# Kernel tuning notes

Measured on AMD Instinct MI355X. Metric: run time of the kernel, lower is better.

Reference implementation:

```python
import jax, jax.numpy as jnp
import numpy as np

N = 40000
E = 640000
IN_C = 128
HID = 256
HEADS = 8


def _gat(x, W, att_src, att_dst, bias, src, dst, num_nodes, heads, concat):
    # x: [N, Fin], W: [Fin, heads*C], att_*: [heads, C], bias: [out_dim]
    xp = (x @ W).reshape(num_nodes, heads, -1)          # [N, H, C]
    a_s = jnp.sum(xp * att_src, axis=-1)                # [N, H]
    a_d = jnp.sum(xp * att_dst, axis=-1)                # [N, H]
    e = jax.nn.leaky_relu(a_s[src] + a_d[dst], 0.2)     # [E, H]
    # per-destination-node softmax over incoming edges (self-loops guarantee >=1)
    m = jax.ops.segment_max(e, dst, num_segments=num_nodes)
    m = jnp.where(jnp.isfinite(m), m, 0.0)
    ex = jnp.exp(e - m[dst])
    denom = jax.ops.segment_sum(ex, dst, num_segments=num_nodes)
    alpha = ex / (denom[dst] + 1e-16)                   # [E, H]
    out = jax.ops.segment_sum(xp[src] * alpha[..., None], dst, num_segments=num_nodes)  # [N,H,C]
    out = out.reshape(num_nodes, -1) if concat else out.mean(axis=1)
    return out + bias


def setup_inputs() -> dict:
    key = jax.random.key(0)
    ks = jax.random.split(key, 16)
    C = HID // HEADS
    s = 0.05
    return {
        "x": jax.random.normal(ks[0], (N, IN_C), jnp.float32),
        "edge_index": jax.random.randint(ks[1], (2, E), 0, N, jnp.int32),
        "W0": jax.random.normal(ks[2], (IN_C, HEADS * C), jnp.float32) * s,
        "att_s0": jax.random.normal(ks[3], (HEADS, C), jnp.float32) * s,
        "att_d0": jax.random.normal(ks[4], (HEADS, C), jnp.float32) * s,
        "b0": jnp.zeros((HID,), jnp.float32),
        # BatchNorm(256)
        "gamma0": jnp.ones((HID,), jnp.float32),
        "beta0": jnp.zeros((HID,), jnp.float32),
        # skip projection Linear(128 -> 256)
        "W_skip": jax.random.normal(ks[5], (IN_C, HID), jnp.float32) * s,
        "b_skip": jnp.zeros((HID,), jnp.float32),
        # last layer: GATConv(256 -> 256, heads=1, concat=False)
        "W1": jax.random.normal(ks[6], (HID, HID), jnp.float32) * s,
        "att_s1": jax.random.normal(ks[7], (1, HID), jnp.float32) * s,
        "att_d1": jax.random.normal(ks[8], (1, HID), jnp.float32) * s,
        "b1": jnp.zeros((HID,), jnp.float32),
    }


def reference(x, edge_index, W0, att_s0, att_d0, b0, gamma0, beta0,
              W_skip, b_skip, W1, att_s1, att_d1, b1):
    loops = jnp.arange(N, dtype=edge_index.dtype)
    src = jnp.concatenate([edge_index[0], loops])
    dst = jnp.concatenate([edge_index[1], loops])
    # conv 0 (heads=8, concat)
    h = _gat(x, W0, att_s0, att_d0, b0, src, dst, N, HEADS, True)
    # BatchNorm (training-style batch stats, biased variance, eps=1e-5)
    mu = h.mean(axis=0)
    var = h.var(axis=0)
    h = (h - mu) / jnp.sqrt(var + 1e-5) * gamma0 + beta0
    h = jax.nn.elu(h)
    # dropout is identity in eval mode
    # residual: shapes differ (128 vs 256) -> skip_proj(x_initial) + h at i==0
    h = h + (x @ W_skip + b_skip)
    # conv 1 (heads=1, concat=False -> mean over single head)
    out = _gat(h, W1, att_s1, att_d1, b1, src, dst, N, 1, False)
    return out
```

## Files before the change

### kernel.cpp

```cpp
#include <hip/hip_runtime.h>
#include <hip/hip_bf16.h>

#define NN 40000
#define EE 640000
#define ET 680000
#define MPAD 40064
#define LOG2E 1.4426950408889634f

typedef __attribute__((ext_vector_type(8))) short short8;
typedef __attribute__((ext_vector_type(4))) float f32x4;

__device__ __forceinline__ float bf2f(unsigned u) {
    return __uint_as_float(u << 16);
}
__device__ __forceinline__ unsigned short f2bf(float f) {
    unsigned u = __float_as_uint(f);
    return (unsigned short)((u + 0x7FFFu + ((u >> 16) & 1u)) >> 16);
}
__device__ __forceinline__ unsigned pack2(float lo, float hi) {
    return ((unsigned)f2bf(lo)) | (((unsigned)f2bf(hi)) << 16);
}
__device__ __forceinline__ void unpack2(unsigned u, float& lo, float& hi) {
    lo = __uint_as_float(u << 16);
    hi = __uint_as_float(u & 0xffff0000u);
}

__global__ __launch_bounds__(256) void conv_x(const float* __restrict__ x,
                                              unsigned short* __restrict__ xb)
{
    int i = blockIdx.x * 256 + threadIdx.x;
    if (i >= MPAD * 128 / 4) return;
    int row = (i * 4) >> 7;
    ushort4 o;
    if (row < NN) {
        float4 v = ((const float4*)x)[i];
        o.x = f2bf(v.x); o.y = f2bf(v.y); o.z = f2bf(v.z); o.w = f2bf(v.w);
    } else { o.x = o.y = o.z = o.w = 0; }
    ((ushort4*)xb)[i] = o;
}

__global__ __launch_bounds__(256) void conv_wt_all(
    const float* __restrict__ W0, const float* __restrict__ Ws,
    const float* __restrict__ W1, unsigned short* __restrict__ Wtc,
    unsigned short* __restrict__ W1t)
{
    int i = blockIdx.x * 256 + threadIdx.x;
    if (i < 32768) {
        int c = i >> 7, k = i & 127;
        Wtc[i] = f2bf(W0[(size_t)k * 256 + c]);
    } else if (i < 65536) {
        int j = i - 32768;
        int c = j >> 7, k = j & 127;
        Wtc[i] = f2bf(Ws[(size_t)k * 256 + c]);
    } else if (i < 131072) {
        int j = i - 65536;
        int c = j >> 8, k = j & 255;
        W1t[j] = f2bf(W1[(size_t)k * 256 + c]);
    }
}

__global__ __launch_bounds__(256) void gemm_bf16(
    const unsigned short* __restrict__ A, const unsigned short* __restrict__ Btc,
    unsigned short* __restrict__ C0, unsigned short* __restrict__ C1, int K)
{
    __shared__ unsigned short As[128 * 64];
    int tid = threadIdx.x;
    int rb = blockIdx.x * 128, cb = blockIdx.y * 128;
    int lane = tid & 63, wid = tid >> 6;
    int wm = (wid >> 1) * 64, wn = (wid & 1) * 64;
    int lr = lane & 15, lk = lane >> 4;
    f32x4 acc[4][4] = {};
    for (int kb = 0; kb < K; kb += 64) {
        #pragma unroll
        for (int i = 0; i < 4; i++) {
            int flat = tid + i * 256;
            int r = flat >> 3, c8 = flat & 7;
            int4 v = *(const int4*)(A + (size_t)(rb + r) * K + kb + c8 * 8);
            *(int4*)(&As[r * 64 + ((c8 ^ (r & 7)) * 8)]) = v;
        }
        __syncthreads();
        #pragma unroll
        for (int kk = 0; kk < 2; kk++) {
            int kbase = kb + kk * 32 + lk * 8;
            short8 bfr[4], afr[4];
            #pragma unroll
            for (int n = 0; n < 4; n++)
                bfr[n] = *(const short8*)(Btc + (size_t)(cb + wn + n * 16 + lr) * K + kbase);
            #pragma unroll
            for (int m = 0; m < 4; m++) {
                int row = wm + m * 16 + lr;
                int kchunk = kk * 4 + lk;
                afr[m] = *(const short8*)(&As[row * 64 + ((kchunk ^ (row & 7)) * 8)]);
            }
            #pragma unroll
            for (int m = 0; m < 4; m++)
                #pragma unroll
                for (int n = 0; n < 4; n++)
                    acc[m][n] = __builtin_amdgcn_mfma_f32_16x16x32_bf16(afr[m], bfr[n], acc[m][n], 0, 0, 0);
        }
        __syncthreads();
    }
    unsigned short* C = (cb < 256) ? C0 : C1;
    int cbase = cb & 255;
    #pragma unroll
    for (int m = 0; m < 4; m++)
        #pragma unroll
        for (int n = 0; n < 4; n++) {
            int col = cbase + wn + n * 16 + lr;
            #pragma unroll
            for (int j = 0; j < 4; j++) {
                int row = rb + wm + m * 16 + lk * 4 + j;
                C[(size_t)row * 256 + col] = f2bf(acc[m][n][j]);
            }
        }
}

__global__ __launch_bounds__(256) void csr_count(const int* __restrict__ ei, int* __restrict__ deg)
{
    int e = blockIdx.x * blockDim.x + threadIdx.x;
    if (e >= ET) return;
    int d = (e < EE) ? ei[EE + e] : (e - EE);
    atomicAdd(&deg[d], 1);
}

__global__ __launch_bounds__(1024) void exscan(
    const int* __restrict__ deg, int* __restrict__ rowptr, int* __restrict__ cursor)
{
    __shared__ int wsum[16];
    __shared__ int carry_s;
    int tid = threadIdx.x, lane = tid & 63, wid = tid >> 6;
    if (tid == 0) carry_s = 0;
    __syncthreads();
    for (int base = 0; base < NN; base += 1024) {
        int i = base + tid;
        int v = (i < NN) ? deg[i] : 0;
        int sc = v;
        #pragma unroll
        for (int off = 1; off < 64; off <<= 1) {
            int t = __shfl_up(sc, off);
            if (lane >= off) sc += t;
        }
        if (lane == 63) wsum[wid] = sc;
        __syncthreads();
        if (wid == 0 && lane < 16) {
            int t = wsum[lane];
            #pragma unroll
            for (int off = 1; off < 16; off <<= 1) {
                int u = __shfl_up(t, off);
                if (lane >= off) t += u;
            }
            wsum[lane] = t;
        }
        __syncthreads();
        int carry = carry_s;
        int wpre = wid ? wsum[wid - 1] : 0;
        int excl = carry + wpre + sc - v;
        if (i < NN) { rowptr[i] = excl; cursor[i] = excl; }
        __syncthreads();
        if (tid == 0) carry_s = carry + wsum[15];
    }
    if (tid == 0) rowptr[NN] = carry_s;
}

__global__ __launch_bounds__(256) void csr_fill(
    const int* __restrict__ ei, int* __restrict__ cursor, int* __restrict__ adj)
{
    int e = blockIdx.x * blockDim.x + threadIdx.x;
    if (e >= ET) return;
    int s, d;
    if (e < EE) { s = ei[e]; d = ei[EE + e]; } else { s = d = e - EE; }
    int pos = atomicAdd(&cursor[d], 1);
    adj[pos] = s;
}

__global__ __launch_bounds__(256) void attn_node0(
    const unsigned short* __restrict__ xp, const float* __restrict__ att_s,
    const float* __restrict__ att_d, float* __restrict__ a_s, float* __restrict__ a_d)
{
    int t = blockIdx.x * 256 + threadIdx.x;
    if (t >= NN * 8) return;
    int n = t >> 3, h = t & 7;
    const unsigned short* p = xp + (size_t)n * 256 + h * 32;
    float s = 0.f, dd = 0.f;
    #pragma unroll
    for (int i0 = 0; i0 < 32; i0 += 8) {
        uint4 raw = *(const uint4*)(p + i0);
        unsigned vals[4] = {raw.x, raw.y, raw.z, raw.w};
        #pragma unroll
        for (int q = 0; q < 4; q++) {
            float lo, hi;
            unpack2(vals[q], lo, hi);
            s  += lo * att_s[h * 32 + i0 + q * 2] + hi * att_s[h * 32 + i0 + q * 2 + 1];
            dd += lo * att_d[h * 32 + i0 + q * 2] + hi * att_d[h * 32 + i0 + q * 2 + 1];
        }
    }
    a_s[t] = s * LOG2E; a_d[t] = dd * LOG2E;
}

__global__ __launch_bounds__(256) void attn_node1(
    const unsigned short* __restrict__ xp, const float* __restrict__ att_s,
    const float* __restrict__ att_d, float* __restrict__ a_s, float* __restrict__ a_d)
{
    int w = (blockIdx.x * 256 + threadIdx.x) >> 6;
    int lane = threadIdx.x & 63;
    if (w >= NN) return;
    ushort4 raw = ((const ushort4*)(xp + (size_t)w * 256))[lane];
    float4 a = ((const float4*)att_s)[lane];
    float4 b = ((const float4*)att_d)[lane];
    float v0 = bf2f(raw.x), v1 = bf2f(raw.y), v2 = bf2f(raw.z), v3 = bf2f(raw.w);
    float s  = v0 * a.x + v1 * a.y + v2 * a.z + v3 * a.w;
    float dd = v0 * b.x + v1 * b.y + v2 * b.z + v3 * b.w;
    #pragma unroll
    for (int off = 32; off; off >>= 1) {
        s  += __shfl_down(s, off);
        dd += __shfl_down(dd, off);
    }
    if (lane == 0) { a_s[w] = s * LOG2E; a_d[w] = dd * LOG2E; }
}

__global__ __launch_bounds__(256) void gather0(
    const int* __restrict__ adj, const int* __restrict__ rowptr,
    const unsigned short* __restrict__ xp, const float* __restrict__ a_s,
    const float* __restrict__ a_d, unsigned short* __restrict__ out0)
{
    int w = (blockIdx.x * 256 + threadIdx.x) >> 6;
    int lane = threadIdx.x & 63;
    if (w >= NN) return;
    int hl = lane & 31;
    int hw = lane >> 5;
    int h = hl >> 2;
    float ad = a_d[w * 8 + h];
    int p = rowptr[w], end = rowptr[w + 1];
    unsigned loff = (unsigned)hl * 16u;
    float a0=0,a1=0,a2=0,a3=0,a4=0,a5=0,a6=0,a7=0;
    float b0=0,b1=0,b2=0,b3=0,b4=0,b5=0,b6=0,b7=0;
    float den0 = 0.f, den1 = 0.f;
    float lo, hi;
    for (; p + 8 <= end; p += 8) {
        int sA = adj[p + hw];
        int sB = adj[p + 2 + hw];
        int sC = adj[p + 4 + hw];
        int sD = adj[p + 6 + hw];
        float eA = a_s[sA * 8 + h] + ad;
        float eB = a_s[sB * 8 + h] + ad;
        float eC = a_s[sC * 8 + h] + ad;
        float eD = a_s[sD * 8 + h] + ad;
        float wA = __builtin_amdgcn_exp2f(fmaxf(eA, 0.2f * eA));
        float wB = __builtin_amdgcn_exp2f(fmaxf(eB, 0.2f * eB));
        float wC = __builtin_amdgcn_exp2f(fmaxf(eC, 0.2f * eC));
        float wD = __builtin_amdgcn_exp2f(fmaxf(eD, 0.2f * eD));
        uint4 rA = *(const uint4*)((const char*)xp + ((unsigned)sA * 512u + loff));
        uint4 rB = *(const uint4*)((const char*)xp + ((unsigned)sB * 512u + loff));
        uint4 rC = *(const uint4*)((const char*)xp + ((unsigned)sC * 512u + loff));
        uint4 rD = *(const uint4*)((const char*)xp + ((unsigned)sD * 512u + loff));
        den0 += wA + wC; den1 += wB + wD;
        unpack2(rA.x, lo, hi); a0 += wA * lo; a1 += wA * hi;
        unpack2(rA.y, lo, hi); a2 += wA * lo; a3 += wA * hi;
        unpack2(rA.z, lo, hi); a4 += wA * lo; a5 += wA * hi;
        unpack2(rA.w, lo, hi); a6 += wA * lo; a7 += wA * hi;
        unpack2(rB.x, lo, hi); b0 += wB * lo; b1 += wB * hi;
        unpack2(rB.y, lo, hi); b2 += wB * lo; b3 += wB * hi;
        unpack2(rB.z, lo, hi); b4 += wB * lo; b5 += wB * hi;
        unpack2(rB.w, lo, hi); b6 += wB * lo; b7 += wB * hi;
        unpack2(rC.x, lo, hi); a0 += wC * lo; a1 += wC * hi;
        unpack2(rC.y, lo, hi); a2 += wC * lo; a3 += wC * hi;
        unpack2(rC.z, lo, hi); a4 += wC * lo; a5 += wC * hi;
        unpack2(rC.w, lo, hi); a6 += wC * lo; a7 += wC * hi;
        unpack2(rD.x, lo, hi); b0 += wD * lo; b1 += wD * hi;
        unpack2(rD.y, lo, hi); b2 += wD * lo; b3 += wD * hi;
        unpack2(rD.z, lo, hi); b4 += wD * lo; b5 += wD * hi;
        unpack2(rD.w, lo, hi); b6 += wD * lo; b7 += wD * hi;
    }
    for (; p + 2 <= end; p += 2) {
        int sA = adj[p + hw];
        float eA = a_s[sA * 8 + h] + ad;
        float wA = __builtin_amdgcn_exp2f(fmaxf(eA, 0.2f * eA));
        uint4 rA = *(const uint4*)((const char*)xp + ((unsigned)sA * 512u + loff));
        den0 += wA;
        unpack2(rA.x, lo, hi); a0 += wA * lo; a1 += wA * hi;
        unpack2(rA.y, lo, hi); a2 += wA * lo; a3 += wA * hi;
        unpack2(rA.z, lo, hi); a4 += wA * lo; a5 += wA * hi;
        unpack2(rA.w, lo, hi); a6 += wA * lo; a7 += wA * hi;
    }
    if (p < end) {
        int sA = adj[p];
        float eA = a_s[sA * 8 + h] + ad;
        float wA = hw ? 0.f : __builtin_amdgcn_exp2f(fmaxf(eA, 0.2f * eA));
        uint4 rA = *(const uint4*)((const char*)xp + ((unsigned)sA * 512u + loff));
        den0 += wA;
        unpack2(rA.x, lo, hi); a0 += wA * lo; a1 += wA * hi;
        unpack2(rA.y, lo, hi); a2 += wA * lo; a3 += wA * hi;
        unpack2(rA.z, lo, hi); a4 += wA * lo; a5 += wA * hi;
        unpack2(rA.w, lo, hi); a6 += wA * lo; a7 += wA * hi;
    }
    a0 += b0; a1 += b1; a2 += b2; a3 += b3;
    a4 += b4; a5 += b5; a6 += b6; a7 += b7;
    float den = den0 + den1;
    den += __shfl_xor(den, 32);
    a0 += __shfl_xor(a0, 32); a1 += __shfl_xor(a1, 32);
    a2 += __shfl_xor(a2, 32); a3 += __shfl_xor(a3, 32);
    a4 += __shfl_xor(a4, 32); a5 += __shfl_xor(a5, 32);
    a6 += __shfl_xor(a6, 32); a7 += __shfl_xor(a7, 32);
    if (hw == 0) {
        float inv = 1.f / (den + 1e-16f);
        uint4 o;
        o.x = pack2(a0 * inv, a1 * inv);
        o.y = pack2(a2 * inv, a3 * inv);
        o.z = pack2(a4 * inv, a5 * inv);
        o.w = pack2(a6 * inv, a7 * inv);
        *(uint4*)((char*)out0 + ((size_t)w * 512u + loff)) = o;
    }
}

__global__ __launch_bounds__(256) void bn_stats(
    const unsigned short* __restrict__ H, float* __restrict__ bnsum, float* __restrict__ bnsq)
{
    int c = threadIdx.x;
    int r0 = blockIdx.x * 64;
    float s = 0.f, sq = 0.f;
    for (int r = r0; r < r0 + 64; r++) {
        float v = bf2f(H[(size_t)r * 256 + c]);
        s += v; sq += v * v;
    }
    atomicAdd(&bnsum[c], s);
    atomicAdd(&bnsq[c], sq);
}

__global__ __launch_bounds__(256) void bn_elu(
    const unsigned short* __restrict__ out0, unsigned short* __restrict__ hb,
    const float* __restrict__ bnsum, const float* __restrict__ bnsq,
    const float* __restrict__ gamma, const float* __restrict__ beta,
    const float* __restrict__ bskip)
{
    int i = blockIdx.x * 256 + threadIdx.x;
    if (i >= MPAD * 256 / 8) return;
    int col0 = (i * 8) & 255;
    uint4 hv = ((const uint4*)out0)[i];
    uint4 sv = ((const uint4*)hb)[i];
    float bn[8], sk[8];
    unpack2(hv.x, bn[0], bn[1]); unpack2(hv.y, bn[2], bn[3]);
    unpack2(hv.z, bn[4], bn[5]); unpack2(hv.w, bn[6], bn[7]);
    unpack2(sv.x, sk[0], sk[1]); unpack2(sv.y, sk[2], sk[3]);
    unpack2(sv.z, sk[4], sk[5]); unpack2(sv.w, sk[6], sk[7]);
    const float invN = 1.0f / (float)NN;
    float r[8];
    #pragma unroll
    for (int q = 0; q < 8; q++) {
        int c = col0 + q;
        float mu = bnsum[c] * invN;
        float var = bnsq[c] * invN - mu * mu;
        float scl = rsqrtf(var + 1e-5f) * gamma[c];
        float b = (bn[q] - mu) * scl + beta[c];
        float el = b > 0.f ? b : (__expf(b) - 1.f);
        r[q] = el + sk[q] + bskip[c];
    }
    uint4 o;
    o.x = pack2(r[0], r[1]); o.y = pack2(r[2], r[3]);
    o.z = pack2(r[4], r[5]); o.w = pack2(r[6], r[7]);
    ((uint4*)hb)[i] = o;
}

__global__ __launch_bounds__(256) void gather1(
    const int* __restrict__ adj, const int* __restrict__ rowptr,
    const unsigned short* __restrict__ xp, const float* __restrict__ a_s,
    const float* __restrict__ a_d, const float* __restrict__ b1,
    float* __restrict__ out)
{
    int w = (blockIdx.x * 256 + threadIdx.x) >> 6;
    int lane = threadIdx.x & 63;
    if (w >= NN) return;
    int hl = lane & 31;
    int hw = lane >> 5;
    float ad = a_d[w];
    int p = rowptr[w], end = rowptr[w + 1];
    unsigned loff = (unsigned)hl * 16u;
    float a0=0,a1=0,a2=0,a3=0,a4=0,a5=0,a6=0,a7=0;
    float b0s=0,b1s=0,b2s=0,b3s=0,b4s=0,b5s=0,b6s=0,b7s=0;
    float den0 = 0.f, den1 = 0.f;
    float lo, hi;
    for (; p + 8 <= end; p += 8) {
        int sA = adj[p + hw];
        int sB = adj[p + 2 + hw];
        int sC = adj[p + 4 + hw];
        int sD = adj[p + 6 + hw];
        float eA = a_s[sA] + ad;
        float eB = a_s[sB] + ad;
        float eC = a_s[sC] + ad;
        float eD = a_s[sD] + ad;
        float wA = __builtin_amdgcn_exp2f(fmaxf(eA, 0.2f * eA));
        float wB = __builtin_amdgcn_exp2f(fmaxf(eB, 0.2f * eB));
        float wC = __builtin_amdgcn_exp2f(fmaxf(eC, 0.2f * eC));
        float wD = __builtin_amdgcn_exp2f(fmaxf(eD, 0.2f * eD));
        uint4 rA = *(const uint4*)((const char*)xp + ((unsigned)sA * 512u + loff));
        uint4 rB = *(const uint4*)((const char*)xp + ((unsigned)sB * 512u + loff));
        uint4 rC = *(const uint4*)((const char*)xp + ((unsigned)sC * 512u + loff));
        uint4 rD = *(const uint4*)((const char*)xp + ((unsigned)sD * 512u + loff));
        den0 += wA + wC; den1 += wB + wD;
        unpack2(rA.x, lo, hi); a0 += wA * lo; a1 += wA * hi;
        unpack2(rA.y, lo, hi); a2 += wA * lo; a3 += wA * hi;
        unpack2(rA.z, lo, hi); a4 += wA * lo; a5 += wA * hi;
        unpack2(rA.w, lo, hi); a6 += wA * lo; a7 += wA * hi;
        unpack2(rB.x, lo, hi); b0s += wB * lo; b1s += wB * hi;
        unpack2(rB.y, lo, hi); b2s += wB * lo; b3s += wB * hi;
        unpack2(rB.z, lo, hi); b4s += wB * lo; b5s += wB * hi;
        unpack2(rB.w, lo, hi); b6s += wB * lo; b7s += wB * hi;
        unpack2(rC.x, lo, hi); a0 += wC * lo; a1 += wC * hi;
        unpack2(rC.y, lo, hi); a2 += wC * lo; a3 += wC * hi;
        unpack2(rC.z, lo, hi); a4 += wC * lo; a5 += wC * hi;
        unpack2(rC.w, lo, hi); a6 += wC * lo; a7 += wC * hi;
        unpack2(rD.x, lo, hi); b0s += wD * lo; b1s += wD * hi;
        unpack2(rD.y, lo, hi); b2s += wD * lo; b3s += wD * hi;
        unpack2(rD.z, lo, hi); b4s += wD * lo; b5s += wD * hi;
        unpack2(rD.w, lo, hi); b6s += wD * lo; b7s += wD * hi;
    }
    for (; p + 2 <= end; p += 2) {
        int sA = adj[p + hw];
        float eA = a_s[sA] + ad;
        float wA = __builtin_amdgcn_exp2f(fmaxf(eA, 0.2f * eA));
        uint4 rA = *(const uint4*)((const char*)xp + ((unsigned)sA * 512u + loff));
        den0 += wA;
        unpack2(rA.x, lo, hi); a0 += wA * lo; a1 += wA * hi;
        unpack2(rA.y, lo, hi); a2 += wA * lo; a3 += wA * hi;
        unpack2(rA.z, lo, hi); a4 += wA * lo; a5 += wA * hi;
        unpack2(rA.w, lo, hi); a6 += wA * lo; a7 += wA * hi;
    }
    if (p < end) {
        int sA = adj[p];
        float eA = a_s[sA] + ad;
        float wA = hw ? 0.f : __builtin_amdgcn_exp2f(fmaxf(eA, 0.2f * eA));
        uint4 rA = *(const uint4*)((const char*)xp + ((unsigned)sA * 512u + loff));
        den0 += wA;
        unpack2(rA.x, lo, hi); a0 += wA * lo; a1 += wA * hi;
        unpack2(rA.y, lo, hi); a2 += wA * lo; a3 += wA * hi;
        unpack2(rA.z, lo, hi); a4 += wA * lo; a5 += wA * hi;
        unpack2(rA.w, lo, hi); a6 += wA * lo; a7 += wA * hi;
    }
    a0 += b0s; a1 += b1s; a2 += b2s; a3 += b3s;
    a4 += b4s; a5 += b5s; a6 += b6s; a7 += b7s;
    float den = den0 + den1;
    den += __shfl_xor(den, 32);
    a0 += __shfl_xor(a0, 32); a1 += __shfl_xor(a1, 32);
    a2 += __shfl_xor(a2, 32); a3 += __shfl_xor(a3, 32);
    a4 += __shfl_xor(a4, 32); a5 += __shfl_xor(a5, 32);
    a6 += __shfl_xor(a6, 32); a7 += __shfl_xor(a7, 32);
    if (hw == 0) {
        float inv = 1.f / (den + 1e-16f);
        const float* bb = b1 + hl * 8;
        float4 o0 = {a0 * inv + bb[0], a1 * inv + bb[1],
                     a2 * inv + bb[2], a3 * inv + bb[3]};
        float4 o1 = {a4 * inv + bb[4], a5 * inv + bb[5],
                     a6 * inv + bb[6], a7 * inv + bb[7]};
        float* orow = out + (size_t)w * 256 + hl * 8;
        *(float4*)(orow) = o0;
        *(float4*)(orow + 4) = o1;
    }
}

extern "C" void kernel_launch(void* const* d_in, const int* in_sizes, int n_in,
                              void* d_out, int out_size, void* d_ws, size_t ws_size,
                              hipStream_t stream)
{
    const float* x      = (const float*)d_in[0];
    const int*   ei     = (const int*)d_in[1];
    const float* W0     = (const float*)d_in[2];
    const float* att_s0 = (const float*)d_in[3];
    const float* att_d0 = (const float*)d_in[4];
    const float* gamma0 = (const float*)d_in[6];
    const float* beta0  = (const float*)d_in[7];
    const float* W_skip = (const float*)d_in[8];
    const float* b_skip = (const float*)d_in[9];
    const float* W1     = (const float*)d_in[10];
    const float* att_s1 = (const float*)d_in[11];
    const float* att_d1 = (const float*)d_in[12];
    const float* b1     = (const float*)d_in[13];
    float* out = (float*)d_out;

    char* p = (char*)d_ws;
    unsigned short* x_bf  = (unsigned short*)p; p += (size_t)MPAD * 128 * 2;
    unsigned short* xp_bf = (unsigned short*)p; p += (size_t)MPAD * 256 * 2;
    unsigned short* h_bf  = (unsigned short*)p; p += (size_t)MPAD * 256 * 2;
    unsigned short* out0b = (unsigned short*)p; p += (size_t)MPAD * 256 * 2;
    unsigned short* Wtc   = (unsigned short*)p; p += (size_t)512 * 128 * 2;
    unsigned short* W1t   = (unsigned short*)p; p += (size_t)256 * 256 * 2;
    float* a_s   = (float*)p; p += (size_t)NN * 8 * 4;
    float* a_d   = (float*)p; p += (size_t)NN * 8 * 4;
    float* bnsum = (float*)p; p += 256 * 4;
    float* bnsq  = (float*)p; p += 256 * 4;
    int* deg    = (int*)p; p += (size_t)NN * 4;
    int* rowptr = (int*)p; p += (size_t)(NN + 1) * 4;
    int* cursor = (int*)p; p += (size_t)NN * 4;
    int* adj    = (int*)p; p += (size_t)ET * 4;

    hipMemsetAsync(deg, 0, (size_t)NN * 4, stream);
    hipMemsetAsync(bnsum, 0, 512 * 4, stream);
    hipMemsetAsync(out0b + (size_t)NN * 256, 0, (size_t)(MPAD - NN) * 256 * 2, stream);

    conv_x<<<(MPAD * 128 / 4 + 255) / 256, 256, 0, stream>>>(x, x_bf);
    conv_wt_all<<<(131072 + 255) / 256, 256, 0, stream>>>(W0, W_skip, W1, Wtc, W1t);

    csr_count<<<(ET + 255) / 256, 256, 0, stream>>>(ei, deg);
    exscan<<<1, 1024, 0, stream>>>(deg, rowptr, cursor);
    csr_fill<<<(ET + 255) / 256, 256, 0, stream>>>(ei, cursor, adj);

    dim3 gg0(MPAD / 128, 4);
    gemm_bf16<<<gg0, 256, 0, stream>>>(x_bf, Wtc, xp_bf, h_bf, 128);
    attn_node0<<<(NN * 8 + 255) / 256, 256, 0, stream>>>(xp_bf, att_s0, att_d0, a_s, a_d);
    gather0<<<(NN * 64 + 255) / 256, 256, 0, stream>>>(adj, rowptr, xp_bf, a_s, a_d, out0b);

    bn_stats<<<NN / 64, 256, 0, stream>>>(out0b, bnsum, bnsq);
    bn_elu<<<(MPAD * 256 / 8 + 255) / 256, 256, 0, stream>>>(out0b, h_bf, bnsum, bnsq,
                                                             gamma0, beta0, b_skip);

    dim3 gg1(MPAD / 128, 2);
    gemm_bf16<<<gg1, 256, 0, stream>>>(h_bf, W1t, xp_bf, xp_bf, 256);
    attn_node1<<<(NN * 64 + 255) / 256, 256, 0, stream>>>(xp_bf, att_s1, att_d1, a_s, a_d);
    gather1<<<(NN * 64 + 255) / 256, 256, 0, stream>>>(adj, rowptr, xp_bf, a_s, a_d, b1, out);
}
```

Measured before the change: 321.6 us.

## Aggregate before projecting in both GAT layers and fold attention into weights

Reorders each GAT layer so neighbor aggregation runs on the narrower input features and the weight projection is applied afterwards. For layer 0 that means gathering 128-wide x rows per head, followed by a per-head GEMM. Attention logits are computed from precomputed W·att vectors (u, v), so the projected features are no longer needed for them. The layer-1 attention dot product is fused into the BN/ELU kernel, and the final GEMM adds the bias and writes the output. Layer 0 now writes an 8x-wide per-head aggregate buffer and does per-head exp work for every edge, which adds memory traffic and ALU work in exchange for smaller gathered rows.

```diff
diff --git a/kernel.cpp b/kernel.cpp
--- a/kernel.cpp
+++ b/kernel.cpp
@@ -39,23 +39,44 @@
     ((ushort4*)xb)[i] = o;
 }
 
-__global__ __launch_bounds__(256) void conv_wt_all(
+__global__ __launch_bounds__(256) void conv_w_all(
     const float* __restrict__ W0, const float* __restrict__ Ws,
-    const float* __restrict__ W1, unsigned short* __restrict__ Wtc,
-    unsigned short* __restrict__ W1t)
+    const float* __restrict__ W1,
+    const float* __restrict__ as0, const float* __restrict__ ad0,
+    const float* __restrict__ as1, const float* __restrict__ ad1,
+    unsigned short* __restrict__ W0t, unsigned short* __restrict__ Wst,
+    unsigned short* __restrict__ W1t, float* __restrict__ u, float* __restrict__ v)
 {
     int i = blockIdx.x * 256 + threadIdx.x;
     if (i < 32768) {
         int c = i >> 7, k = i & 127;
-        Wtc[i] = f2bf(W0[(size_t)k * 256 + c]);
+        W0t[i] = f2bf(W0[(size_t)k * 256 + c]);
     } else if (i < 65536) {
         int j = i - 32768;
         int c = j >> 7, k = j & 127;
-        Wtc[i] = f2bf(Ws[(size_t)k * 256 + c]);
+        Wst[j] = f2bf(Ws[(size_t)k * 256 + c]);
     } else if (i < 131072) {
         int j = i - 65536;
         int c = j >> 8, k = j & 255;
         W1t[j] = f2bf(W1[(size_t)k * 256 + c]);
+    } else if (i < 133120) {
+        int j = i - 131072;
+        int k = j >> 4, jj = j & 15;
+        int h = jj & 7;
+        const float* att = (jj < 8) ? as0 : ad0;
+        float sum = 0.f;
+        #pragma unroll
+        for (int c = 0; c < 32; c++)
+            sum += W0[(size_t)k * 256 + h * 32 + c] * att[h * 32 + c];
+        u[j] = sum * LOG2E;
+    } else if (i < 133632) {
+        int j = i - 133120;
+        int k = j >> 1, which = j & 1;
+        const float* att = which ? ad1 : as1;
+        float sum = 0.f;
+        for (int c = 0; c < 256; c++)
+            sum += W1[(size_t)k * 256 + c] * att[c];
+        v[j] = sum * LOG2E;
     }
 }
 
@@ -113,6 +134,115 @@
                 C[(size_t)row * 256 + col] = f2bf(acc[m][n][j]);
             }
         }
+}
+
+__global__ __launch_bounds__(256) void gemm_agg0(
+    const unsigned short* __restrict__ agg, const unsigned short* __restrict__ W0t,
+    unsigned short* __restrict__ C)
+{
+    __shared__ unsigned short As[128 * 128];
+    int tid = threadIdx.x;
+    int rb = blockIdx.x * 128;
+    int hb = blockIdx.y;
+    int lane = tid & 63, wid = tid >> 6;
+    int lr = lane & 15, lk = lane >> 4;
+    #pragma unroll
+    for (int i = 0; i < 8; i++) {
+        int flat = tid + i * 256;
+        int r = flat >> 4, c8 = flat & 15;
+        int4 v = *(const int4*)(agg + (size_t)(rb + r) * 1024 + hb * 128 + c8 * 8);
+        *(int4*)(&As[r * 128 + ((c8 ^ (r & 7)) * 8)]) = v;
+    }
+    __syncthreads();
+    f32x4 acc[2][2] = {};
+    int wm = wid * 32;
+    #pragma unroll
+    for (int kk = 0; kk < 4; kk++) {
+        int kbase = kk * 32 + lk * 8;
+        short8 bfr[2], afr[2];
+        #pragma unroll
+        for (int n = 0; n < 2; n++)
+            bfr[n] = *(const short8*)(W0t + (size_t)(hb * 32 + n * 16 + lr) * 128 + kbase);
+        #pragma unroll
+        for (int m = 0; m < 2; m++) {
+            int row = wm + m * 16 + lr;
+            int ck = kk * 4 + lk;
+            afr[m] = *(const short8*)(&As[row * 128 + ((ck ^ (row & 7)) * 8)]);
+        }
+        #pragma unroll
+        for (int m = 0; m < 2; m++)
+            #pragma unroll
+            for (int n = 0; n < 2; n++)
+                acc[m][n] = __builtin_amdgcn_mfma_f32_16x16x32_bf16(afr[m], bfr[n], acc[m][n], 0, 0, 0);
+    }
+    #pragma unroll
+    for (int m = 0; m < 2; m++)
+        #pragma unroll
+        for (int n = 0; n < 2; n++) {
+            int col = hb * 32 + n * 16 + lr;
+            #pragma unroll
+            for (int j = 0; j < 4; j++) {
+                int row = rb + wm + m * 16 + lk * 4 + j;
+                C[(size_t)row * 256 + col] = f2bf(acc[m][n][j]);
+            }
+        }
+}
+
+__global__ __launch_bounds__(256) void gemm_final(
+    const unsigned short* __restrict__ A, const unsigned short* __restrict__ Btc,
+    const float* __restrict__ b1, float* __restrict__ out)
+{
+    __shared__ unsigned short As[128 * 64];
+    const int K = 256;
+    int tid = threadIdx.x;
+    int rb = blockIdx.x * 128, cb = blockIdx.y * 128;
+    int lane = tid & 63, wid = tid >> 6;
+    int wm = (wid >> 1) * 64, wn = (wid & 1) * 64;
+    int lr = lane & 15, lk = lane >> 4;
+    f32x4 acc[4][4] = {};
+    for (int kb = 0; kb < K; kb += 64) {
+        #pragma unroll
+        for (int i = 0; i < 4; i++) {
+            int flat = tid + i * 256;
+            int r = flat >> 3, c8 = flat & 7;
+            int4 v = *(const int4*)(A + (size_t)(rb + r) * K + kb + c8 * 8);
+            *(int4*)(&As[r * 64 + ((c8 ^ (r & 7)) * 8)]) = v;
+        }
+        __syncthreads();
+        #pragma unroll
+        for (int kk = 0; kk < 2; kk++) {
+            int kbase = kb + kk * 32 + lk * 8;
+            short8 bfr[4], afr[4];
+            #pragma unroll
+            for (int n = 0; n < 4; n++)
+                bfr[n] = *(const short8*)(Btc + (size_t)(cb + wn + n * 16 + lr) * K + kbase);
+            #pragma unroll
+            for (int m = 0; m < 4; m++) {
+                int row = wm + m * 16 + lr;
+                int kchunk = kk * 4 + lk;
+                afr[m] = *(const short8*)(&As[row * 64 + ((kchunk ^ (row & 7)) * 8)]);
+            }
+            #pragma unroll
+            for (int m = 0; m < 4; m++)
+                #pragma unroll
+                for (int n = 0; n < 4; n++)
+                    acc[m][n] = __builtin_amdgcn_mfma_f32_16x16x32_bf16(afr[m], bfr[n], acc[m][n], 0, 0, 0);
+        }
+        __syncthreads();
+    }
+    #pragma unroll
+    for (int n = 0; n < 4; n++) {
+        int col = cb + wn + n * 16 + lr;
+        float bc = b1[col];
+        #pragma unroll
+        for (int m = 0; m < 4; m++)
+            #pragma unroll
+            for (int j = 0; j < 4; j++) {
+                int row = rb + wm + m * 16 + lk * 4 + j;
+                if (row < NN)
+                    out[(size_t)row * 256 + col] = acc[m][n][j] + bc;
+            }
+    }
 }
 
 __global__ __launch_bounds__(256) void csr_count(const int* __restrict__ ei, int* __restrict__ deg)
@@ -173,109 +303,216 @@
     adj[pos] = s;
 }
 
-__global__ __launch_bounds__(256) void attn_node0(
-    const unsigned short* __restrict__ xp, const float* __restrict__ att_s,
-    const float* __restrict__ att_d, float* __restrict__ a_s, float* __restrict__ a_d)
-{
-    int t = blockIdx.x * 256 + threadIdx.x;
-    if (t >= NN * 8) return;
-    int n = t >> 3, h = t & 7;
-    const unsigned short* p = xp + (size_t)n * 256 + h * 32;
-    float s = 0.f, dd = 0.f;
-    #pragma unroll
-    for (int i0 = 0; i0 < 32; i0 += 8) {
-        uint4 raw = *(const uint4*)(p + i0);
-        unsigned vals[4] = {raw.x, raw.y, raw.z, raw.w};
-        #pragma unroll
-        for (int q = 0; q < 4; q++) {
-            float lo, hi;
-            unpack2(vals[q], lo, hi);
-            s  += lo * att_s[h * 32 + i0 + q * 2] + hi * att_s[h * 32 + i0 + q * 2 + 1];
-            dd += lo * att_d[h * 32 + i0 + q * 2] + hi * att_d[h * 32 + i0 + q * 2 + 1];
-        }
-    }
-    a_s[t] = s * LOG2E; a_d[t] = dd * LOG2E;
-}
-
-__global__ __launch_bounds__(256) void attn_node1(
-    const unsigned short* __restrict__ xp, const float* __restrict__ att_s,
-    const float* __restrict__ att_d, float* __restrict__ a_s, float* __restrict__ a_d)
+__global__ __launch_bounds__(256) void attn0(
+    const unsigned short* __restrict__ xb, const float* __restrict__ u,
+    float* __restrict__ a_s, float* __restrict__ a_d)
 {
     int w = (blockIdx.x * 256 + threadIdx.x) >> 6;
     int lane = threadIdx.x & 63;
     if (w >= NN) return;
-    ushort4 raw = ((const ushort4*)(xp + (size_t)w * 256))[lane];
-    float4 a = ((const float4*)att_s)[lane];
-    float4 b = ((const float4*)att_d)[lane];
-    float v0 = bf2f(raw.x), v1 = bf2f(raw.y), v2 = bf2f(raw.z), v3 = bf2f(raw.w);
-    float s  = v0 * a.x + v1 * a.y + v2 * a.z + v3 * a.w;
-    float dd = v0 * b.x + v1 * b.y + v2 * b.z + v3 * b.w;
-    #pragma unroll
-    for (int off = 32; off; off >>= 1) {
-        s  += __shfl_down(s, off);
-        dd += __shfl_down(dd, off);
-    }
-    if (lane == 0) { a_s[w] = s * LOG2E; a_d[w] = dd * LOG2E; }
-}
-
-__global__ __launch_bounds__(256) void gather0(
+    unsigned r = *(const unsigned*)(xb + (size_t)w * 128 + lane * 2);
+    float x0, x1;
+    unpack2(r, x0, x1);
+    const float* u0 = u + (lane * 2) * 16;
+    const float* u1 = u0 + 16;
+    float ps[8], pd[8];
+    #pragma unroll
+    for (int h = 0; h < 8; h++) {
+        ps[h] = x0 * u0[h] + x1 * u1[h];
+        pd[h] = x0 * u0[8 + h] + x1 * u1[8 + h];
+    }
+    #pragma unroll
+    for (int off = 1; off < 64; off <<= 1) {
+        #pragma unroll
+        for (int h = 0; h < 8; h++) {
+            ps[h] += __shfl_xor(ps[h], off);
+            pd[h] += __shfl_xor(pd[h], off);
+        }
+    }
+    if (lane == 0) {
+        #pragma unroll
+        for (int h = 0; h < 8; h++) {
+            a_s[w * 8 + h] = ps[h];
+            a_d[w * 8 + h] = pd[h];
+        }
+    }
+}
+
+__global__ __launch_bounds__(256) void gather0p(
     const int* __restrict__ adj, const int* __restrict__ rowptr,
-    const unsigned short* __restrict__ xp, const float* __restrict__ a_s,
-    const float* __restrict__ a_d, unsigned short* __restrict__ out0)
+    const unsigned short* __restrict__ xb, const float* __restrict__ a_s,
+    const float* __restrict__ a_d, unsigned short* __restrict__ agg)
+{
+    int w = (blockIdx.x * 256 + threadIdx.x) >> 6;
+    int lane = threadIdx.x & 63;
+    if (w >= NN) return;
+    int hl = lane & 31, hw = lane >> 5;
+    float4 adl0 = *(const float4*)(a_d + w * 8);
+    float4 adl1 = *(const float4*)(a_d + w * 8 + 4);
+    float ad[8] = {adl0.x, adl0.y, adl0.z, adl0.w, adl1.x, adl1.y, adl1.z, adl1.w};
+    int p = rowptr[w], end = rowptr[w + 1];
+    unsigned loff = (unsigned)hl * 8u;
+    float acc[8][4] = {};
+    float den[8] = {};
+    for (; p + 2 <= end; p += 2) {
+        int s = adj[p + hw];
+        float4 as0 = *(const float4*)(a_s + s * 8);
+        float4 as1 = *(const float4*)(a_s + s * 8 + 4);
+        float as[8] = {as0.x, as0.y, as0.z, as0.w, as1.x, as1.y, as1.z, as1.w};
+        uint2 r = *(const uint2*)((const char*)xb + ((unsigned)s * 256u + loff));
+        float c0, c1, c2, c3;
+        unpack2(r.x, c0, c1); unpack2(r.y, c2, c3);
+        #pragma unroll
+        for (int h = 0; h < 8; h++) {
+            float e = as[h] + ad[h];
+            float wt = __builtin_amdgcn_exp2f(fmaxf(e, 0.2f * e));
+            den[h] += wt;
+            acc[h][0] += wt * c0; acc[h][1] += wt * c1;
+            acc[h][2] += wt * c2; acc[h][3] += wt * c3;
+        }
+    }
+    if (p < end) {
+        int s = adj[p];
+        float4 as0 = *(const float4*)(a_s + s * 8);
+        float4 as1 = *(const float4*)(a_s + s * 8 + 4);
+        float as[8] = {as0.x, as0.y, as0.z, as0.w, as1.x, as1.y, as1.z, as1.w};
+        uint2 r = *(const uint2*)((const char*)xb + ((unsigned)s * 256u + loff));
+        float c0, c1, c2, c3;
+        unpack2(r.x, c0, c1); unpack2(r.y, c2, c3);
+        float m = hw ? 0.f : 1.f;
+        #pragma unroll
+        for (int h = 0; h < 8; h++) {
+            float e = as[h] + ad[h];
+            float wt = m * __builtin_amdgcn_exp2f(fmaxf(e, 0.2f * e));
+            den[h] += wt;
+            acc[h][0] += wt * c0; acc[h][1] += wt * c1;
+            acc[h][2] += wt * c2; acc[h][3] += wt * c3;
+        }
+    }
+    #pragma unroll
+    for (int h = 0; h < 8; h++) {
+        den[h] += __shfl_xor(den[h], 32);
+        acc[h][0] += __shfl_xor(acc[h][0], 32);
+        acc[h][1] += __shfl_xor(acc[h][1], 32);
+        acc[h][2] += __shfl_xor(acc[h][2], 32);
+        acc[h][3] += __shfl_xor(acc[h][3], 32);
+    }
+    if (hw == 0) {
+        #pragma unroll
+        for (int h = 0; h < 8; h++) {
+            float inv = 1.f / (den[h] + 1e-16f);
+            uint2 o;
+            o.x = pack2(acc[h][0] * inv, acc[h][1] * inv);
+            o.y = pack2(acc[h][2] * inv, acc[h][3] * inv);
+            *(uint2*)((char*)agg + ((size_t)w * 2048u + h * 256u + loff)) = o;
+        }
+    }
+}
+
+__global__ __launch_bounds__(256) void bn_stats(
+    const unsigned short* __restrict__ H, float* __restrict__ bnsum, float* __restrict__ bnsq)
+{
+    int c = threadIdx.x;
+    int r0 = blockIdx.x * 64;
+    float s = 0.f, sq = 0.f;
+    for (int r = r0; r < r0 + 64; r++) {
+        float v = bf2f(H[(size_t)r * 256 + c]);
+        s += v; sq += v * v;
+    }
+    atomicAdd(&bnsum[c], s);
+    atomicAdd(&bnsq[c], sq);
+}
+
+__global__ __launch_bounds__(256) void bn_elu_attn(
+    const unsigned short* __restrict__ out0, unsigned short* __restrict__ hb,
+    const float* __restrict__ bnsum, const float* __restrict__ bnsq,
+    const float* __restrict__ gamma, const float* __restrict__ beta,
+    const float* __restrict__ bskip, const float* __restrict__ v,
+    float* __restrict__ a_s, float* __restrict__ a_d)
+{
+    int i = blockIdx.x * 256 + threadIdx.x;
+    if (i >= MPAD * 32) return;
+    int col0 = (i * 8) & 255;
+    int row = i >> 5;
+    uint4 hv = ((const uint4*)out0)[i];
+    uint4 sv = ((const uint4*)hb)[i];
+    float bn[8], sk[8];
+    unpack2(hv.x, bn[0], bn[1]); unpack2(hv.y, bn[2], bn[3]);
+    unpack2(hv.z, bn[4], bn[5]); unpack2(hv.w, bn[6], bn[7]);
+    unpack2(sv.x, sk[0], sk[1]); unpack2(sv.y, sk[2], sk[3]);
+    unpack2(sv.z, sk[4], sk[5]); unpack2(sv.w, sk[6], sk[7]);
+    const float invN = 1.0f / (float)NN;
+    float r[8];
+    float ps = 0.f, pd = 0.f;
+    #pragma unroll
+    for (int q = 0; q < 8; q++) {
+        int c = col0 + q;
+        float mu = bnsum[c] * invN;
+        float var = bnsq[c] * invN - mu * mu;
+        float scl = rsqrtf(var + 1e-5f) * gamma[c];
+        float b = (bn[q] - mu) * scl + beta[c];
+        float el = b > 0.f ? b : (__expf(b) - 1.f);
+        r[q] = el + sk[q] + bskip[c];
+        float2 vv = *(const float2*)(v + c * 2);
+        ps += r[q] * vv.x;
+        pd += r[q] * vv.y;
+    }
+    uint4 o;
+    o.x = pack2(r[0], r[1]); o.y = pack2(r[2], r[3]);
+    o.z = pack2(r[4], r[5]); o.w = pack2(r[6], r[7]);
+    ((uint4*)hb)[i] = o;
+    #pragma unroll
+    for (int off = 1; off < 32; off <<= 1) {
+        ps += __shfl_xor(ps, off);
+        pd += __shfl_xor(pd, off);
+    }
+    if ((threadIdx.x & 31) == 0 && row < NN) {
+        a_s[row] = ps;
+        a_d[row] = pd;
+    }
+}
+
+__global__ __launch_bounds__(256) void gather1p(
+    const int* __restrict__ adj, const int* __restrict__ rowptr,
+    const unsigned short* __restrict__ hbuf, const float* __restrict__ a_s,
+    const float* __restrict__ a_d, unsigned short* __restrict__ agg1)
 {
     int w = (blockIdx.x * 256 + threadIdx.x) >> 6;
     int lane = threadIdx.x & 63;
     if (w >= NN) return;
     int hl = lane & 31;
     int hw = lane >> 5;
-    int h = hl >> 2;
-    float ad = a_d[w * 8 + h];
+    float ad = a_d[w];
     int p = rowptr[w], end = rowptr[w + 1];
     unsigned loff = (unsigned)hl * 16u;
     float a0=0,a1=0,a2=0,a3=0,a4=0,a5=0,a6=0,a7=0;
-    float b0=0,b1=0,b2=0,b3=0,b4=0,b5=0,b6=0,b7=0;
+    float b0=0,b1s=0,b2=0,b3=0,b4=0,b5=0,b6=0,b7=0;
     float den0 = 0.f, den1 = 0.f;
     float lo, hi;
-    for (; p + 8 <= end; p += 8) {
+    for (; p + 4 <= end; p += 4) {
         int sA = adj[p + hw];
         int sB = adj[p + 2 + hw];
-        int sC = adj[p + 4 + hw];
-        int sD = adj[p + 6 + hw];
-        float eA = a_s[sA * 8 + h] + ad;
-        float eB = a_s[sB * 8 + h] + ad;
-        float eC = a_s[sC * 8 + h] + ad;
-        float eD = a_s[sD * 8 + h] + ad;
+        float eA = a_s[sA] + ad;
+        float eB = a_s[sB] + ad;
         float wA = __builtin_amdgcn_exp2f(fmaxf(eA, 0.2f * eA));
         float wB = __builtin_amdgcn_exp2f(fmaxf(eB, 0.2f * eB));
-        float wC = __builtin_amdgcn_exp2f(fmaxf(eC, 0.2f * eC));
-        float wD = __builtin_amdgcn_exp2f(fmaxf(eD, 0.2f * eD));
-        uint4 rA = *(const uint4*)((const char*)xp + ((unsigned)sA * 512u + loff));
-        uint4 rB = *(const uint4*)((const char*)xp + ((unsigned)sB * 512u + loff));
-        uint4 rC = *(const uint4*)((const char*)xp + ((unsigned)sC * 512u + loff));
-        uint4 rD = *(const uint4*)((const char*)xp + ((unsigned)sD * 512u + loff));
-        den0 += wA + wC; den1 += wB + wD;
+        uint4 rA = *(const uint4*)((const char*)hbuf + ((unsigned)sA * 512u + loff));
+        uint4 rB = *(const uint4*)((const char*)hbuf + ((unsigned)sB * 512u + loff));
+        den0 += wA; den1 += wB;
         unpack2(rA.x, lo, hi); a0 += wA * lo; a1 += wA * hi;
         unpack2(rA.y, lo, hi); a2 += wA * lo; a3 += wA * hi;
         unpack2(rA.z, lo, hi); a4 += wA * lo; a5 += wA * hi;
         unpack2(rA.w, lo, hi); a6 += wA * lo; a7 += wA * hi;
-        unpack2(rB.x, lo, hi); b0 += wB * lo; b1 += wB * hi;
+        unpack2(rB.x, lo, hi); b0 += wB * lo; b1s += wB * hi;
         unpack2(rB.y, lo, hi); b2 += wB * lo; b3 += wB * hi;
         unpack2(rB.z, lo, hi); b4 += wB * lo; b5 += wB * hi;
         unpack2(rB.w, lo, hi); b6 += wB * lo; b7 += wB * hi;
-        unpack2(rC.x, lo, hi); a0 += wC * lo; a1 += wC * hi;
-        unpack2(rC.y, lo, hi); a2 += wC * lo; a3 += wC * hi;
-        unpack2(rC.z, lo, hi); a4 += wC * lo; a5 += wC * hi;
-        unpack2(rC.w, lo, hi); a6 += wC * lo; a7 += wC * hi;
-        unpack2(rD.x, lo, hi); b0 += wD * lo; b1 += wD * hi;
-        unpack2(rD.y, lo, hi); b2 += wD * lo; b3 += wD * hi;
-        unpack2(rD.z, lo, hi); b4 += wD * lo; b5 += wD * hi;
-        unpack2(rD.w, lo, hi); b6 += wD * lo; b7 += wD * hi;
     }
     for (; p + 2 <= end; p += 2) {
         int sA = adj[p + hw];
-        float eA = a_s[sA * 8 + h] + ad;
+        float eA = a_s[sA] + ad;
         float wA = __builtin_amdgcn_exp2f(fmaxf(eA, 0.2f * eA));
-        uint4 rA = *(const uint4*)((const char*)xp + ((unsigned)sA * 512u + loff));
+        uint4 rA = *(const uint4*)((const char*)hbuf + ((unsigned)sA * 512u + loff));
         den0 += wA;
         unpack2(rA.x, lo, hi); a0 += wA * lo; a1 += wA * hi;
         unpack2(rA.y, lo, hi); a2 += wA * lo; a3 += wA * hi;
@@ -284,16 +521,16 @@
     }
     if (p < end) {
         int sA = adj[p];
-        float eA = a_s[sA * 8 + h] + ad;
+        float eA = a_s[sA] + ad;
         float wA = hw ? 0.f : __builtin_amdgcn_exp2f(fmaxf(eA, 0.2f * eA));
-        uint4 rA = *(const uint4*)((const char*)xp + ((unsigned)sA * 512u + loff));
+        uint4 rA = *(const uint4*)((const char*)hbuf + ((unsigned)sA * 512u + loff));
         den0 += wA;
         unpack2(rA.x, lo, hi); a0 += wA * lo; a1 += wA * hi;
         unpack2(rA.y, lo, hi); a2 += wA * lo; a3 += wA * hi;
         unpack2(rA.z, lo, hi); a4 += wA * lo; a5 += wA * hi;
         unpack2(rA.w, lo, hi); a6 += wA * lo; a7 += wA * hi;
     }
-    a0 += b0; a1 += b1; a2 += b2; a3 += b3;
+    a0 += b0; a1 += b1s; a2 += b2; a3 += b3;
     a4 += b4; a5 += b5; a6 += b6; a7 += b7;
     float den = den0 + den1;
     den += __shfl_xor(den, 32);
@@ -308,151 +545,7 @@
         o.y = pack2(a2 * inv, a3 * inv);
         o.z = pack2(a4 * inv, a5 * inv);
         o.w = pack2(a6 * inv, a7 * inv);
-        *(uint4*)((char*)out0 + ((size_t)w * 512u + loff)) = o;
-    }
-}
-
-__global__ __launch_bounds__(256) void bn_stats(
-    const unsigned short* __restrict__ H, float* __restrict__ bnsum, float* __restrict__ bnsq)
-{
-    int c = threadIdx.x;
-    int r0 = blockIdx.x * 64;
-    float s = 0.f, sq = 0.f;
-    for (int r = r0; r < r0 + 64; r++) {
-        float v = bf2f(H[(size_t)r * 256 + c]);
-        s += v; sq += v * v;
-    }
-    atomicAdd(&bnsum[c], s);
-    atomicAdd(&bnsq[c], sq);
-}
-
-__global__ __launch_bounds__(256) void bn_elu(
-    const unsigned short* __restrict__ out0, unsigned short* __restrict__ hb,
-    const float* __restrict__ bnsum, const float* __restrict__ bnsq,
-    const float* __restrict__ gamma, const float* __restrict__ beta,
-    const float* __restrict__ bskip)
-{
-    int i = blockIdx.x * 256 + threadIdx.x;
-    if (i >= MPAD * 256 / 8) return;
-    int col0 = (i * 8) & 255;
-    uint4 hv = ((const uint4*)out0)[i];
-    uint4 sv = ((const uint4*)hb)[i];
-    float bn[8], sk[8];
-    unpack2(hv.x, bn[0], bn[1]); unpack2(hv.y, bn[2], bn[3]);
-    unpack2(hv.z, bn[4], bn[5]); unpack2(hv.w, bn[6], bn[7]);
-    unpack2(sv.x, sk[0], sk[1]); unpack2(sv.y, sk[2], sk[3]);
-    unpack2(sv.z, sk[4], sk[5]); unpack2(sv.w, sk[6], sk[7]);
-    const float invN = 1.0f / (float)NN;
-    float r[8];
-    #pragma unroll
-    for (int q = 0; q < 8; q++) {
-        int c = col0 + q;
-        float mu = bnsum[c] * invN;
-        float var = bnsq[c] * invN - mu * mu;
-        float scl = rsqrtf(var + 1e-5f) * gamma[c];
-        float b = (bn[q] - mu) * scl + beta[c];
-        float el = b > 0.f ? b : (__expf(b) - 1.f);
-        r[q] = el + sk[q] + bskip[c];
-    }
-    uint4 o;
-    o.x = pack2(r[0], r[1]); o.y = pack2(r[2], r[3]);
-    o.z = pack2(r[4], r[5]); o.w = pack2(r[6], r[7]);
-    ((uint4*)hb)[i] = o;
-}
-
-__global__ __launch_bounds__(256) void gather1(
-    const int* __restrict__ adj, const int* __restrict__ rowptr,
-    const unsigned short* __restrict__ xp, const float* __restrict__ a_s,
-    const float* __restrict__ a_d, const float* __restrict__ b1,
-    float* __restrict__ out)
-{
-    int w = (blockIdx.x * 256 + threadIdx.x) >> 6;
-    int lane = threadIdx.x & 63;
-    if (w >= NN) return;
-    int hl = lane & 31;
-    int hw = lane >> 5;
-    float ad = a_d[w];
-    int p = rowptr[w], end = rowptr[w + 1];
-    unsigned loff = (unsigned)hl * 16u;
-    float a0=0,a1=0,a2=0,a3=0,a4=0,a5=0,a6=0,a7=0;
-    float b0s=0,b1s=0,b2s=0,b3s=0,b4s=0,b5s=0,b6s=0,b7s=0;
-    float den0 = 0.f, den1 = 0.f;
-    float lo, hi;
-    for (; p + 8 <= end; p += 8) {
-        int sA = adj[p + hw];
-        int sB = adj[p + 2 + hw];
-        int sC = adj[p + 4 + hw];
-        int sD = adj[p + 6 + hw];
-        float eA = a_s[sA] + ad;
-        float eB = a_s[sB] + ad;
-        float eC = a_s[sC] + ad;
-        float eD = a_s[sD] + ad;
-        float wA = __builtin_amdgcn_exp2f(fmaxf(eA, 0.2f * eA));
-        float wB = __builtin_amdgcn_exp2f(fmaxf(eB, 0.2f * eB));
-        float wC = __builtin_amdgcn_exp2f(fmaxf(eC, 0.2f * eC));
-        float wD = __builtin_amdgcn_exp2f(fmaxf(eD, 0.2f * eD));
-        uint4 rA = *(const uint4*)((const char*)xp + ((unsigned)sA * 512u + loff));
-        uint4 rB = *(const uint4*)((const char*)xp + ((unsigned)sB * 512u + loff));
-        uint4 rC = *(const uint4*)((const char*)xp + ((unsigned)sC * 512u + loff));
-        uint4 rD = *(const uint4*)((const char*)xp + ((unsigned)sD * 512u + loff));
-        den0 += wA + wC; den1 += wB + wD;
-        unpack2(rA.x, lo, hi); a0 += wA * lo; a1 += wA * hi;
-        unpack2(rA.y, lo, hi); a2 += wA * lo; a3 += wA * hi;
-        unpack2(rA.z, lo, hi); a4 += wA * lo; a5 += wA * hi;
-        unpack2(rA.w, lo, hi); a6 += wA * lo; a7 += wA * hi;
-        unpack2(rB.x, lo, hi); b0s += wB * lo; b1s += wB * hi;
-        unpack2(rB.y, lo, hi); b2s += wB * lo; b3s += wB * hi;
-        unpack2(rB.z, lo, hi); b4s += wB * lo; b5s += wB * hi;
-        unpack2(rB.w, lo, hi); b6s += wB * lo; b7s += wB * hi;
-        unpack2(rC.x, lo, hi); a0 += wC * lo; a1 += wC * hi;
-        unpack2(rC.y, lo, hi); a2 += wC * lo; a3 += wC * hi;
-        unpack2(rC.z, lo, hi); a4 += wC * lo; a5 += wC * hi;
-        unpack2(rC.w, lo, hi); a6 += wC * lo; a7 += wC * hi;
-        unpack2(rD.x, lo, hi); b0s += wD * lo; b1s += wD * hi;
-        unpack2(rD.y, lo, hi); b2s += wD * lo; b3s += wD * hi;
-        unpack2(rD.z, lo, hi); b4s += wD * lo; b5s += wD * hi;
-        unpack2(rD.w, lo, hi); b6s += wD * lo; b7s += wD * hi;
-    }
-    for (; p + 2 <= end; p += 2) {
-        int sA = adj[p + hw];
-        float eA = a_s[sA] + ad;
-        float wA = __builtin_amdgcn_exp2f(fmaxf(eA, 0.2f * eA));
-        uint4 rA = *(const uint4*)((const char*)xp + ((unsigned)sA * 512u + loff));
-        den0 += wA;
-        unpack2(rA.x, lo, hi); a0 += wA * lo; a1 += wA * hi;
-        unpack2(rA.y, lo, hi); a2 += wA * lo; a3 += wA * hi;
-        unpack2(rA.z, lo, hi); a4 += wA * lo; a5 += wA * hi;
-        unpack2(rA.w, lo, hi); a6 += wA * lo; a7 += wA * hi;
-    }
-    if (p < end) {
-        int sA = adj[p];
-        float eA = a_s[sA] + ad;
-        float wA = hw ? 0.f : __builtin_amdgcn_exp2f(fmaxf(eA, 0.2f * eA));
-        uint4 rA = *(const uint4*)((const char*)xp + ((unsigned)sA * 512u + loff));
-        den0 += wA;
-        unpack2(rA.x, lo, hi); a0 += wA * lo; a1 += wA * hi;
-        unpack2(rA.y, lo, hi); a2 += wA * lo; a3 += wA * hi;
-        unpack2(rA.z, lo, hi); a4 += wA * lo; a5 += wA * hi;
-        unpack2(rA.w, lo, hi); a6 += wA * lo; a7 += wA * hi;
-    }
-    a0 += b0s; a1 += b1s; a2 += b2s; a3 += b3s;
-    a4 += b4s; a5 += b5s; a6 += b6s; a7 += b7s;
-    float den = den0 + den1;
-    den += __shfl_xor(den, 32);
-    a0 += __shfl_xor(a0, 32); a1 += __shfl_xor(a1, 32);
-    a2 += __shfl_xor(a2, 32); a3 += __shfl_xor(a3, 32);
-    a4 += __shfl_xor(a4, 32); a5 += __shfl_xor(a5, 32);
-    a6 += __shfl_xor(a6, 32); a7 += __shfl_xor(a7, 32);
-    if (hw == 0) {
-        float inv = 1.f / (den + 1e-16f);
-        const float* bb = b1 + hl * 8;
-        float4 o0 = {a0 * inv + bb[0], a1 * inv + bb[1],
-                     a2 * inv + bb[2], a3 * inv + bb[3]};
-        float4 o1 = {a4 * inv + bb[4], a5 * inv + bb[5],
-                     a6 * inv + bb[6], a7 * inv + bb[7]};
-        float* orow = out + (size_t)w * 256 + hl * 8;
-        *(float4*)(orow) = o0;
-        *(float4*)(orow + 4) = o1;
+        *(uint4*)((char*)agg1 + ((size_t)w * 512u + loff)) = o;
     }
 }
 
@@ -477,11 +570,15 @@
 
     char* p = (char*)d_ws;
     unsigned short* x_bf  = (unsigned short*)p; p += (size_t)MPAD * 128 * 2;
-    unsigned short* xp_bf = (unsigned short*)p; p += (size_t)MPAD * 256 * 2;
     unsigned short* h_bf  = (unsigned short*)p; p += (size_t)MPAD * 256 * 2;
     unsigned short* out0b = (unsigned short*)p; p += (size_t)MPAD * 256 * 2;
-    unsigned short* Wtc   = (unsigned short*)p; p += (size_t)512 * 128 * 2;
-    unsigned short* W1t   = (unsigned short*)p; p += (size_t)256 * 256 * 2;
+    unsigned short* agg   = (unsigned short*)p; p += (size_t)MPAD * 1024 * 2;
+    unsigned short* agg1  = agg;
+    unsigned short* W0t = (unsigned short*)p; p += (size_t)256 * 128 * 2;
+    unsigned short* Wst = (unsigned short*)p; p += (size_t)256 * 128 * 2;
+    unsigned short* W1t = (unsigned short*)p; p += (size_t)256 * 256 * 2;
+    float* u     = (float*)p; p += 2048 * 4;
+    float* v     = (float*)p; p += 512 * 4;
     float* a_s   = (float*)p; p += (size_t)NN * 8 * 4;
     float* a_d   = (float*)p; p += (size_t)NN * 8 * 4;
     float* bnsum = (float*)p; p += 256 * 4;
@@ -493,26 +590,28 @@
 
     hipMemsetAsync(deg, 0, (size_t)NN * 4, stream);
     hipMemsetAsync(bnsum, 0, 512 * 4, stream);
-    hipMemsetAsync(out0b + (size_t)NN * 256, 0, (size_t)(MPAD - NN) * 256 * 2, stream);
 
     conv_x<<<(MPAD * 128 / 4 + 255) / 256, 256, 0, stream>>>(x, x_bf);
-    conv_wt_all<<<(131072 + 255) / 256, 256, 0, stream>>>(W0, W_skip, W1, Wtc, W1t);
+    conv_w_all<<<(133632 + 255) / 256, 256, 0, stream>>>(
+        W0, W_skip, W1, att_s0, att_d0, att_s1, att_d1, W0t, Wst, W1t, u, v);
 
     csr_count<<<(ET + 255) / 256, 256, 0, stream>>>(ei, deg);
     exscan<<<1, 1024, 0, stream>>>(deg, rowptr, cursor);
     csr_fill<<<(ET + 255) / 256, 256, 0, stream>>>(ei, cursor, adj);
 
-    dim3 gg0(MPAD / 128, 4);
-    gemm_bf16<<<gg0, 256, 0, stream>>>(x_bf, Wtc, xp_bf, h_bf, 128);
-    attn_node0<<<(NN * 8 + 255) / 256, 256, 0, stream>>>(xp_bf, att_s0, att_d0, a_s, a_d);
-    gather0<<<(NN * 64 + 255) / 256, 256, 0, stream>>>(adj, rowptr, xp_bf, a_s, a_d, out0b);
+    attn0<<<(NN * 64 + 255) / 256, 256, 0, stream>>>(x_bf, u, a_s, a_d);
+    gather0p<<<(NN * 64 + 255) / 256, 256, 0, stream>>>(adj, rowptr, x_bf, a_s, a_d, agg);
+    dim3 ga(MPAD / 128, 8);
+    gemm_agg0<<<ga, 256, 0, stream>>>(agg, W0t, out0b);
+
+    dim3 gs(MPAD / 128, 2);
+    gemm_bf16<<<gs, 256, 0, stream>>>(x_bf, Wst, h_bf, h_bf, 128);
 
     bn_stats<<<NN / 64, 256, 0, stream>>>(out0b, bnsum, bnsq);
-    bn_elu<<<(MPAD * 256 / 8 + 255) / 256, 256, 0, stream>>>(out0b, h_bf, bnsum, bnsq,
-                                                             gamma0, beta0, b_skip);
-
-    dim3 gg1(MPAD / 128, 2);
-    gemm_bf16<<<gg1, 256, 0, stream>>>(h_bf, W1t, xp_bf, xp_bf, 256);
-    attn_node1<<<(NN * 64 + 255) / 256, 256, 0, stream>>>(xp_bf, att_s1, att_d1, a_s, a_d);
-    gather1<<<(NN * 64 + 255) / 256, 256, 0, stream>>>(adj, rowptr, xp_bf, a_s, a_d, b1, out);
-}
+    bn_elu_attn<<<(MPAD * 32 + 255) / 256, 256, 0, stream>>>(
+        out0b, h_bf, bnsum, bnsq, gamma0, beta0, b_skip, v, a_s, a_d);
+
+    gather1p<<<(NN * 64 + 255) / 256, 256, 0, stream>>>(adj, rowptr, h_bf, a_s, a_d, agg1);
+    dim3 gf(MPAD / 128, 2);
+    gemm_final<<<gf, 256, 0, stream>>>(agg1, W1t, b1, out);
+}
```

Result: slower. 408.7 us (+27.1%).
